# Kernel tuning notes

Hardware: AMD Instinct MI355X
Metric: run time of the kernel (lower is better)

The kernel has to match this reference:

```python
import jax, jax.numpy as jnp
import numpy as np

N_NODES = 100000
N_MOTIFS = 1000000
R_DIM = 1
D_DIM = 64
N_GRAPHS = 128


def setup_inputs() -> dict:
    key = jax.random.key(0)
    ks = jax.random.split(key, 8)
    Q3 = jax.random.normal(ks[0], (N_NODES, R_DIM, D_DIM), dtype=jnp.float32)
    K3 = jax.random.normal(ks[1], (N_NODES, R_DIM, D_DIM), dtype=jnp.float32)
    T_tau_selected = jax.random.normal(ks[2], (N_MOTIFS, R_DIM, D_DIM), dtype=jnp.float32)
    c_3 = jax.random.randint(ks[3], (N_MOTIFS,), 0, N_NODES, dtype=jnp.int32)
    u_3 = jax.random.randint(ks[4], (N_MOTIFS,), 0, N_NODES, dtype=jnp.int32)
    v_3 = jax.random.randint(ks[5], (N_MOTIFS,), 0, N_NODES, dtype=jnp.int32)
    batch = jnp.sort(jax.random.randint(ks[6], (N_NODES,), 0, N_GRAPHS, dtype=jnp.int32))
    lambda_3 = jnp.ones((1,), dtype=jnp.float32)
    beta_3 = jnp.ones((1,), dtype=jnp.float32)
    return {
        "Q3": Q3, "K3": K3, "T_tau_selected": T_tau_selected,
        "lambda_3": lambda_3, "beta_3": beta_3,
        "c_3": c_3, "u_3": u_3, "v_3": v_3, "batch": batch,
        "num_nodes": N_NODES, "num_graphs": N_GRAPHS,
    }


def reference(Q3, K3, T_tau_selected, lambda_3, beta_3, c_3, u_3, v_3, batch, num_nodes, num_graphs):
    R, d = Q3.shape[-2], Q3.shape[-1]
    scale = float((R * d) ** 0.5)
    lam = lambda_3[0]
    beta = beta_3[0]
    # gather triplet embeddings: [M, R, d]
    q = Q3[c_3]
    ku = K3[u_3]
    kv = K3[v_3]
    # fused motif dot: ell[m] = sum_{r,d} q * (ku*kv + T) / sqrt(R*d)
    ell = jnp.sum(q * (ku * kv + T_tau_selected), axis=(-2, -1)) / scale  # [M]
    bell = beta * ell
    # two-pass segment logsumexp per center node (empty nodes -> 0, as in chunked path)
    seg_max = jax.ops.segment_max(bell, c_3, num_segments=num_nodes)  # identity fill for empty
    max_safe = jnp.where(jnp.isfinite(seg_max), seg_max, 0.0)
    sum_exp = jax.ops.segment_sum(jnp.exp(bell - max_safe[c_3]), c_3, num_segments=num_nodes)
    nonempty = sum_exp > 0
    safe_sum = jnp.where(nonempty, sum_exp, 1.0)
    lse = jnp.where(nonempty, jnp.log(safe_sum) + max_safe, 0.0)  # [N]
    # scatter-add node lse to per-graph energy
    graph_lse = jax.ops.segment_sum(lse, batch, num_segments=num_graphs)  # [G]
    return lam / beta * graph_lse
```

## Files before the change

### kernel.cpp

```cpp
#include <hip/hip_runtime.h>
#include <math.h>


typedef float    f32x4 __attribute__((ext_vector_type(4)));
typedef float    f32x2 __attribute__((ext_vector_type(2)));
typedef unsigned u32x2 __attribute__((ext_vector_type(2)));

__global__ void zero_kernel(float* __restrict__ node_sum, int N,
                            float* __restrict__ out, int G) {
    int i = blockIdx.x * blockDim.x + threadIdx.x;
    if (i < N) node_sum[i] = 0.0f;
    if (i < G) out[i] = 0.0f;
}

__global__ __launch_bounds__(256) void prep_kernel(
    const f32x4* __restrict__ Q4, const f32x4* __restrict__ K4,
    u32x2* __restrict__ Qf, u32x2* __restrict__ Kf, int n8)
{
    int i = blockIdx.x * blockDim.x + threadIdx.x;
    if (i >= n8) return;
    f32x4 a = __builtin_nontemporal_load(&Q4[2 * i]);
    f32x4 b = __builtin_nontemporal_load(&Q4[2 * i + 1]);
    u32x2 w;
    int lo = __builtin_amdgcn_cvt_pk_fp8_f32(a.x, a.y, 0, false);
    lo     = __builtin_amdgcn_cvt_pk_fp8_f32(a.z, a.w, lo, true);
    int hi = __builtin_amdgcn_cvt_pk_fp8_f32(b.x, b.y, 0, false);
    hi     = __builtin_amdgcn_cvt_pk_fp8_f32(b.z, b.w, hi, true);
    w.x = (unsigned)lo; w.y = (unsigned)hi;
    Qf[i] = w;

    a = __builtin_nontemporal_load(&K4[2 * i]);
    b = __builtin_nontemporal_load(&K4[2 * i + 1]);
    lo = __builtin_amdgcn_cvt_pk_fp8_f32(a.x, a.y, 0, false);
    lo = __builtin_amdgcn_cvt_pk_fp8_f32(a.z, a.w, lo, true);
    hi = __builtin_amdgcn_cvt_pk_fp8_f32(b.x, b.y, 0, false);
    hi = __builtin_amdgcn_cvt_pk_fp8_f32(b.z, b.w, hi, true);
    w.x = (unsigned)lo; w.y = (unsigned)hi;
    Kf[i] = w;
}

__global__ __launch_bounds__(256) void motif_kernel(
    const u32x2* __restrict__ Qf, const u32x2* __restrict__ Kf,
    const f32x4* __restrict__ T4, const float* __restrict__ beta_p,
    const int* __restrict__ c3, const int* __restrict__ u3,
    const int* __restrict__ v3, float* __restrict__ node_sum,
    int M, float inv_scale)
{
    long long tid = (long long)blockIdx.x * 256 + threadIdx.x;
    int m = (int)(tid >> 3);
    int g = (int)(tid & 7);
    if (m >= M) return;

    int c = c3[m];
    int u = u3[m];
    int v = v3[m];

    const f32x4* tp = T4 + (size_t)m * 16 + g * 2;
    f32x4 t0 = __builtin_nontemporal_load(tp);
    f32x4 t1 = __builtin_nontemporal_load(tp + 1);

    u32x2 qw  = Qf[(size_t)c * 8 + g];
    u32x2 kuw = Kf[(size_t)u * 8 + g];
    u32x2 kvw = Kf[(size_t)v * 8 + g];

    f32x2 q01  = __builtin_amdgcn_cvt_pk_f32_fp8((int)qw.x,  false);
    f32x2 q23  = __builtin_amdgcn_cvt_pk_f32_fp8((int)qw.x,  true);
    f32x2 q45  = __builtin_amdgcn_cvt_pk_f32_fp8((int)qw.y,  false);
    f32x2 q67  = __builtin_amdgcn_cvt_pk_f32_fp8((int)qw.y,  true);
    f32x2 ku01 = __builtin_amdgcn_cvt_pk_f32_fp8((int)kuw.x, false);
    f32x2 ku23 = __builtin_amdgcn_cvt_pk_f32_fp8((int)kuw.x, true);
    f32x2 ku45 = __builtin_amdgcn_cvt_pk_f32_fp8((int)kuw.y, false);
    f32x2 ku67 = __builtin_amdgcn_cvt_pk_f32_fp8((int)kuw.y, true);
    f32x2 kv01 = __builtin_amdgcn_cvt_pk_f32_fp8((int)kvw.x, false);
    f32x2 kv23 = __builtin_amdgcn_cvt_pk_f32_fp8((int)kvw.x, true);
    f32x2 kv45 = __builtin_amdgcn_cvt_pk_f32_fp8((int)kvw.y, false);
    f32x2 kv67 = __builtin_amdgcn_cvt_pk_f32_fp8((int)kvw.y, true);

    float p =
        q01.x * fmaf(ku01.x, kv01.x, t0.x)
      + q01.y * fmaf(ku01.y, kv01.y, t0.y)
      + q23.x * fmaf(ku23.x, kv23.x, t0.z)
      + q23.y * fmaf(ku23.y, kv23.y, t0.w)
      + q45.x * fmaf(ku45.x, kv45.x, t1.x)
      + q45.y * fmaf(ku45.y, kv45.y, t1.y)
      + q67.x * fmaf(ku67.x, kv67.x, t1.z)
      + q67.y * fmaf(ku67.y, kv67.y, t1.w);

    #pragma unroll
    for (int off = 4; off > 0; off >>= 1)
        p += __shfl_xor(p, off);

    if (g == 0) {
        float bell = beta_p[0] * p * inv_scale;
        atomicAdd(&node_sum[c], __expf(bell));
    }
}

__global__ __launch_bounds__(256) void node_kernel(
    const float* __restrict__ node_sum, const int* __restrict__ batch,
    const float* __restrict__ lam_p, const float* __restrict__ beta_p,
    float* __restrict__ out, int N, int G)
{
    extern __shared__ float gacc[];
    for (int j = threadIdx.x; j < G; j += blockDim.x) gacc[j] = 0.0f;
    __syncthreads();

    int i = blockIdx.x * blockDim.x + threadIdx.x;
    if (i < N) {
        float s = node_sum[i];
        if (s > 0.0f) {
            atomicAdd(&gacc[batch[i]], logf(s));
        }
    }
    __syncthreads();

    float coef = lam_p[0] / beta_p[0];
    for (int j = threadIdx.x; j < G; j += blockDim.x) {
        float v = gacc[j];
        if (v != 0.0f) atomicAdd(&out[j], coef * v);
    }
}

extern "C" void kernel_launch(void* const* d_in, const int* in_sizes, int n_in,
                              void* d_out, int out_size, void* d_ws, size_t ws_size,
                              hipStream_t stream) {
    const float* Q    = (const float*)d_in[0];
    const float* K    = (const float*)d_in[1];
    const float* T    = (const float*)d_in[2];
    const float* lam  = (const float*)d_in[3];
    const float* beta = (const float*)d_in[4];
    const int* c3     = (const int*)d_in[5];
    const int* u3     = (const int*)d_in[6];
    const int* v3     = (const int*)d_in[7];
    const int* batch  = (const int*)d_in[8];

    const int M = in_sizes[5];
    const int N = in_sizes[8];
    const int G = out_size;
    const int RD = in_sizes[0] / N;
    const int n8 = in_sizes[0] / 8;
    const float inv_scale = 1.0f / sqrtf((float)RD);

    float* node_sum = (float*)d_ws;
    size_t off = (((size_t)N * sizeof(float)) + 1023) & ~(size_t)1023;
    u32x2* Qf = (u32x2*)((char*)d_ws + off);
    u32x2* Kf = Qf + n8;
    float* out = (float*)d_out;

    int zmax = (N > G) ? N : G;
    zero_kernel<<<(zmax + 255) / 256, 256, 0, stream>>>(node_sum, N, out, G);

    prep_kernel<<<(n8 + 255) / 256, 256, 0, stream>>>(
        (const f32x4*)Q, (const f32x4*)K, Qf, Kf, n8);

    long long total_threads = (long long)M * 8;
    int mgrid = (int)((total_threads + 255) / 256);
    motif_kernel<<<mgrid, 256, 0, stream>>>(
        Qf, Kf, (const f32x4*)T, beta, c3, u3, v3, node_sum, M, inv_scale);

    node_kernel<<<(N + 255) / 256, 256, G * sizeof(float), stream>>>(
        node_sum, batch, lam, beta, out, N, G);
}
```

Before: 110.5 us.

## Process two motifs per 8-lane group and interleave T column layout

Each 8-thread group now handles two motifs, issuing both motifs' index, T and gathered fp8 loads before computing, which raises memory-level parallelism per thread and halves the grid. The T and Q/K element mapping changes from contiguous 8-float chunks per lane to a strided layout (lane g reads float4 g and g+8), so a group's loads for a motif cover adjacent 16-byte segments per instruction. The prep kernel uses the same permutation so the dot product stays consistent. Register use goes up, and the dot-product sum order changes slightly.

New measurement: 110.0 us. About the same (-0.5%).

```diff
diff --git a/kernel.cpp b/kernel.cpp
--- a/kernel.cpp
+++ b/kernel.cpp
@@ -15,54 +15,37 @@
 
 __global__ __launch_bounds__(256) void prep_kernel(
     const f32x4* __restrict__ Q4, const f32x4* __restrict__ K4,
-    u32x2* __restrict__ Qf, u32x2* __restrict__ Kf, int n8)
+    u32x2* __restrict__ Qf, u32x2* __restrict__ Kf, int nt)
 {
-    int i = blockIdx.x * blockDim.x + threadIdx.x;
-    if (i >= n8) return;
-    f32x4 a = __builtin_nontemporal_load(&Q4[2 * i]);
-    f32x4 b = __builtin_nontemporal_load(&Q4[2 * i + 1]);
+    int t = blockIdx.x * blockDim.x + threadIdx.x;
+    if (t >= nt) return;
+    int r = t >> 3;
+    int g = t & 7;
+    size_t base = (size_t)r * 16 + g;
+
+    f32x4 a = __builtin_nontemporal_load(&Q4[base]);
+    f32x4 b = __builtin_nontemporal_load(&Q4[base + 8]);
     u32x2 w;
     int lo = __builtin_amdgcn_cvt_pk_fp8_f32(a.x, a.y, 0, false);
     lo     = __builtin_amdgcn_cvt_pk_fp8_f32(a.z, a.w, lo, true);
     int hi = __builtin_amdgcn_cvt_pk_fp8_f32(b.x, b.y, 0, false);
     hi     = __builtin_amdgcn_cvt_pk_fp8_f32(b.z, b.w, hi, true);
     w.x = (unsigned)lo; w.y = (unsigned)hi;
-    Qf[i] = w;
+    Qf[(size_t)r * 8 + g] = w;
 
-    a = __builtin_nontemporal_load(&K4[2 * i]);
-    b = __builtin_nontemporal_load(&K4[2 * i + 1]);
+    a = __builtin_nontemporal_load(&K4[base]);
+    b = __builtin_nontemporal_load(&K4[base + 8]);
     lo = __builtin_amdgcn_cvt_pk_fp8_f32(a.x, a.y, 0, false);
     lo = __builtin_amdgcn_cvt_pk_fp8_f32(a.z, a.w, lo, true);
     hi = __builtin_amdgcn_cvt_pk_fp8_f32(b.x, b.y, 0, false);
     hi = __builtin_amdgcn_cvt_pk_fp8_f32(b.z, b.w, hi, true);
     w.x = (unsigned)lo; w.y = (unsigned)hi;
-    Kf[i] = w;
+    Kf[(size_t)r * 8 + g] = w;
 }
 
-__global__ __launch_bounds__(256) void motif_kernel(
-    const u32x2* __restrict__ Qf, const u32x2* __restrict__ Kf,
-    const f32x4* __restrict__ T4, const float* __restrict__ beta_p,
-    const int* __restrict__ c3, const int* __restrict__ u3,
-    const int* __restrict__ v3, float* __restrict__ node_sum,
-    int M, float inv_scale)
+__device__ __forceinline__ float motif_dot(
+    u32x2 qw, u32x2 kuw, u32x2 kvw, f32x4 t0, f32x4 t1)
 {
-    long long tid = (long long)blockIdx.x * 256 + threadIdx.x;
-    int m = (int)(tid >> 3);
-    int g = (int)(tid & 7);
-    if (m >= M) return;
-
-    int c = c3[m];
-    int u = u3[m];
-    int v = v3[m];
-
-    const f32x4* tp = T4 + (size_t)m * 16 + g * 2;
-    f32x4 t0 = __builtin_nontemporal_load(tp);
-    f32x4 t1 = __builtin_nontemporal_load(tp + 1);
-
-    u32x2 qw  = Qf[(size_t)c * 8 + g];
-    u32x2 kuw = Kf[(size_t)u * 8 + g];
-    u32x2 kvw = Kf[(size_t)v * 8 + g];
-
     f32x2 q01  = __builtin_amdgcn_cvt_pk_f32_fp8((int)qw.x,  false);
     f32x2 q23  = __builtin_amdgcn_cvt_pk_f32_fp8((int)qw.x,  true);
     f32x2 q45  = __builtin_amdgcn_cvt_pk_f32_fp8((int)qw.y,  false);
@@ -76,23 +59,66 @@
     f32x2 kv45 = __builtin_amdgcn_cvt_pk_f32_fp8((int)kvw.y, false);
     f32x2 kv67 = __builtin_amdgcn_cvt_pk_f32_fp8((int)kvw.y, true);
 
-    float p =
-        q01.x * fmaf(ku01.x, kv01.x, t0.x)
-      + q01.y * fmaf(ku01.y, kv01.y, t0.y)
-      + q23.x * fmaf(ku23.x, kv23.x, t0.z)
-      + q23.y * fmaf(ku23.y, kv23.y, t0.w)
-      + q45.x * fmaf(ku45.x, kv45.x, t1.x)
-      + q45.y * fmaf(ku45.y, kv45.y, t1.y)
-      + q67.x * fmaf(ku67.x, kv67.x, t1.z)
-      + q67.y * fmaf(ku67.y, kv67.y, t1.w);
+    return q01.x * fmaf(ku01.x, kv01.x, t0.x)
+         + q01.y * fmaf(ku01.y, kv01.y, t0.y)
+         + q23.x * fmaf(ku23.x, kv23.x, t0.z)
+         + q23.y * fmaf(ku23.y, kv23.y, t0.w)
+         + q45.x * fmaf(ku45.x, kv45.x, t1.x)
+         + q45.y * fmaf(ku45.y, kv45.y, t1.y)
+         + q67.x * fmaf(ku67.x, kv67.x, t1.z)
+         + q67.y * fmaf(ku67.y, kv67.y, t1.w);
+}
+
+__global__ __launch_bounds__(256) void motif_kernel(
+    const u32x2* __restrict__ Qf, const u32x2* __restrict__ Kf,
+    const f32x4* __restrict__ T4, const float* __restrict__ beta_p,
+    const int* __restrict__ c3, const int* __restrict__ u3,
+    const int* __restrict__ v3, float* __restrict__ node_sum,
+    int M, float inv_scale)
+{
+    long long tid = (long long)blockIdx.x * 256 + threadIdx.x;
+    int pi = (int)(tid >> 3);
+    int g  = (int)(tid & 7);
+    int m0 = 2 * pi;
+    if (m0 >= M) return;
+    int m1 = m0 + 1;
+    bool has1 = (m1 < M);
+
+    int c0 = c3[m0], u0 = u3[m0], v0 = v3[m0];
+    int c1 = c0, u1 = u0, v1 = v0;
+    if (has1) { c1 = c3[m1]; u1 = u3[m1]; v1 = v3[m1]; }
+
+    const f32x4* tp0 = T4 + (size_t)m0 * 16 + g;
+    f32x4 t00 = __builtin_nontemporal_load(tp0);
+    f32x4 t01 = __builtin_nontemporal_load(tp0 + 8);
+    u32x2 qw0  = Qf[(size_t)c0 * 8 + g];
+    u32x2 kuw0 = Kf[(size_t)u0 * 8 + g];
+    u32x2 kvw0 = Kf[(size_t)v0 * 8 + g];
+
+    f32x4 t10 = t00, t11 = t01;
+    u32x2 qw1 = qw0, kuw1 = kuw0, kvw1 = kvw0;
+    if (has1) {
+        const f32x4* tp1 = T4 + (size_t)m1 * 16 + g;
+        t10 = __builtin_nontemporal_load(tp1);
+        t11 = __builtin_nontemporal_load(tp1 + 8);
+        qw1  = Qf[(size_t)c1 * 8 + g];
+        kuw1 = Kf[(size_t)u1 * 8 + g];
+        kvw1 = Kf[(size_t)v1 * 8 + g];
+    }
+
+    float p0 = motif_dot(qw0, kuw0, kvw0, t00, t01);
+    float p1 = motif_dot(qw1, kuw1, kvw1, t10, t11);
 
     #pragma unroll
-    for (int off = 4; off > 0; off >>= 1)
-        p += __shfl_xor(p, off);
+    for (int off = 4; off > 0; off >>= 1) {
+        p0 += __shfl_xor(p0, off);
+        p1 += __shfl_xor(p1, off);
+    }
 
     if (g == 0) {
-        float bell = beta_p[0] * p * inv_scale;
-        atomicAdd(&node_sum[c], __expf(bell));
+        float bs = beta_p[0] * inv_scale;
+        atomicAdd(&node_sum[c0], __expf(bs * p0));
+        if (has1) atomicAdd(&node_sum[c1], __expf(bs * p1));
     }
 }
 
@@ -138,22 +164,23 @@
     const int N = in_sizes[8];
     const int G = out_size;
     const int RD = in_sizes[0] / N;
-    const int n8 = in_sizes[0] / 8;
+    const int nt = in_sizes[0] / 8;
     const float inv_scale = 1.0f / sqrtf((float)RD);
 
     float* node_sum = (float*)d_ws;
     size_t off = (((size_t)N * sizeof(float)) + 1023) & ~(size_t)1023;
     u32x2* Qf = (u32x2*)((char*)d_ws + off);
-    u32x2* Kf = Qf + n8;
+    u32x2* Kf = Qf + nt;
     float* out = (float*)d_out;
 
     int zmax = (N > G) ? N : G;
     zero_kernel<<<(zmax + 255) / 256, 256, 0, stream>>>(node_sum, N, out, G);
 
-    prep_kernel<<<(n8 + 255) / 256, 256, 0, stream>>>(
-        (const f32x4*)Q, (const f32x4*)K, Qf, Kf, n8);
+    prep_kernel<<<(nt + 255) / 256, 256, 0, stream>>>(
+        (const f32x4*)Q, (const f32x4*)K, Qf, Kf, nt);
 
-    long long total_threads = (long long)M * 8;
+    long long pairs = (M + 1) / 2;
+    long long total_threads = pairs * 8;
     int mgrid = (int)((total_threads + 255) / 256);
     motif_kernel<<<mgrid, 256, 0, stream>>>(
         Qf, Kf, (const f32x4*)T, beta, c3, u3, v3, node_sum, M, inv_scale);
```
